# Optimization experiments

Measured on AMD Instinct MI355X. Metric: run time of the kernel, lower is better.

Reference implementation:

```python
import jax, jax.numpy as jnp
import numpy as np

B, P, K = 32, 2048, 16
NHID, NCLS = 128, 10

def setup_inputs() -> dict:
    key = jax.random.key(0)
    ks = jax.random.split(key, 8)
    def w(k, shape):
        fan_in = shape[0]
        return jax.random.normal(k, shape, jnp.float32) / np.sqrt(fan_in)
    pos = jax.random.normal(ks[0], (B * P, 3), jnp.float32)
    batch = jnp.repeat(jnp.arange(B, dtype=jnp.int32), P)
    return dict(
        pos=pos, batch=batch,
        W1a=w(ks[1], (3 + 3, NHID)), b1a=jnp.zeros((NHID,), jnp.float32),
        W1b=w(ks[2], (NHID, NHID)), b1b=jnp.zeros((NHID,), jnp.float32),
        W2a=w(ks[3], (NHID + 3, NHID)), b2a=jnp.zeros((NHID,), jnp.float32),
        W2b=w(ks[4], (NHID, NHID)), b2b=jnp.zeros((NHID,), jnp.float32),
        Wc=w(ks[5], (NHID, NCLS)), bc=jnp.zeros((NCLS,), jnp.float32),
    )

def _gather(x, idx):
    # x: [B,P,C], idx: [B,P,K] -> [B,P,K,C]
    return jax.vmap(lambda xb, ib: xb[ib])(x, idx)

def _knn(posb):
    # posb: [B,P,3]; k nearest (incl. self, loop=True) per node -> [B,P,K]
    sq = jnp.sum(posb * posb, axis=-1)                      # [B,P]
    d2 = sq[:, :, None] + sq[:, None, :] - 2.0 * jnp.einsum('bpd,bqd->bpq', posb, posb)
    _, nbr = jax.lax.top_k(-d2, K)                          # [B,P,K]
    return nbr

def _pointnet_layer(h, posb, nbr, Wa, ba, Wb, bb):
    # message: concat(h_j, pos_j - pos_i) -> Linear -> ReLU -> Linear; aggr = max over K
    h_j = _gather(h, nbr)                                   # [B,P,K,C]
    rel = _gather(posb, nbr) - posb[:, :, None, :]          # [B,P,K,3]
    m = jnp.concatenate([h_j, rel], axis=-1)                # [B,P,K,C+3]
    m = jax.nn.relu(jnp.einsum('bpkc,cd->bpkd', m, Wa) + ba)
    m = jnp.einsum('bpkc,cd->bpkd', m, Wb) + bb
    return jnp.max(m, axis=2)                               # [B,P,NHID]

def reference(pos, batch, W1a, b1a, W1b, b1b, W2a, b2a, W2b, b2b, Wc, bc):
    posb = pos.reshape(B, P, 3)                             # batch is sorted, equal-size graphs
    nbr = _knn(posb)
    h = jax.nn.relu(_pointnet_layer(posb, posb, nbr, W1a, b1a, W1b, b1b))
    h = jax.nn.relu(_pointnet_layer(h, posb, nbr, W2a, b2a, W2b, b2b))
    g = jnp.max(h, axis=1)                                  # global_max_pool -> [B,NHID]
    return g @ Wc + bc                                      # [B,NCLS]
```

## Files before the change

kernel.cpp:

```cpp
#include <hip/hip_runtime.h>


typedef __bf16 bf16x8 __attribute__((ext_vector_type(8)));
typedef float  f32x4  __attribute__((ext_vector_type(4)));

#define LDSA __attribute__((aligned(16)))
#define WAVE_LDS_SYNC() __asm__ volatile("s_waitcnt lgkmcnt(0)" ::: "memory")

__global__ __launch_bounds__(512, 4) void knn_kernel(const float* __restrict__ pos,
                                                     int* __restrict__ nbr) {
  __shared__ LDSA float4 P4[2048];
  const int blk = blockIdx.x;
  const int b = blk >> 5;
  const int tid = threadIdx.x;
  const size_t bbase = (size_t)b * 2048;
  for (int idx = tid; idx < 2048; idx += 512) {
    const float* pp = pos + (bbase + idx) * 3;
    float x = pp[0], y = pp[1], z = pp[2];
    P4[idx] = make_float4(x, y, z, fmaf(z, z, fmaf(y, y, x * x)));
  }
  __syncthreads();
  const int wave = tid >> 6, lane = tid & 63;
  const int p0 = (blk & 31) * 64 + wave * 8;
  const unsigned long long below = (1ull << lane) - 1ull;
  const float FINF = __uint_as_float(0x7F800000u);
  for (int it = 0; it < 8; ++it) {
    const int pl = p0 + it;
    const float4 P = P4[pl];
    float m1 = FINF, m2 = FINF, m3 = FINF, m4 = FINF;
    unsigned s1 = 0, s2 = 0;
#pragma unroll 8
    for (int i = 0; i < 32; ++i) {
      int c = lane + (i << 6);
      float4 Q = P4[c];
      float d2 = (P.w + Q.w) - 2.0f * fmaf(P.z, Q.z, fmaf(P.y, Q.y, P.x * Q.x));
      bool c1 = d2 < m1, c2 = d2 < m2;
      float nm4 = __builtin_amdgcn_fmed3f(m3, m4, d2);
      float nm3 = __builtin_amdgcn_fmed3f(m2, m3, d2);
      float nm2 = __builtin_amdgcn_fmed3f(m1, m2, d2);
      float nm1 = fminf(m1, d2);
      s2 = c1 ? s1 : (c2 ? (unsigned)c : s2);
      s1 = c1 ? (unsigned)c : s1;
      m1 = nm1; m2 = nm2; m3 = nm3; m4 = nm4;
    }
    unsigned k1 = __float_as_uint(m1); k1 = ((int)k1 < 0) ? ~k1 : (k1 | 0x80000000u);
    unsigned k2 = __float_as_uint(m2); k2 = ((int)k2 < 0) ? ~k2 : (k2 | 0x80000000u);
    unsigned k3 = __float_as_uint(m3); k3 = ((int)k3 < 0) ? ~k3 : (k3 | 0x80000000u);
    unsigned k4 = __float_as_uint(m4); k4 = ((int)k4 < 0) ? ~k4 : (k4 | 0x80000000u);
    unsigned v = 0;
#pragma unroll
    for (int bit = 31; bit >= 0; --bit) {
      unsigned t = v | (1u << bit);
      int cnt = __popcll(__ballot(k1 < t)) + __popcll(__ballot(k2 < t)) +
                __popcll(__ballot(k3 < t));
      if (cnt < 16) v = t;
    }
    const unsigned V = v;
    unsigned s3 = 0;
    if (__any(k3 <= V)) {
      const unsigned m3b = __float_as_uint(m3);
#pragma unroll 8
      for (int i = 0; i < 32; ++i) {
        int c = lane + (i << 6);
        float4 Q = P4[c];
        float d2 = (P.w + Q.w) - 2.0f * fmaf(P.z, Q.z, fmaf(P.y, Q.y, P.x * Q.x));
        if (__float_as_uint(d2) == m3b) s3 = (unsigned)c;
      }
    }
    const long long outbase = ((long long)bbase + pl) * 16;
    if (__any(k4 < V)) {
      unsigned long long K1 = ((unsigned long long)k1 << 32) | s1;
      unsigned long long K2 = ((unsigned long long)k2 << 32) | s2;
      unsigned long long K3 = ((unsigned long long)k3 << 32) | s3;
      unsigned long long lastk = 0;
      for (int r = 0; r < 16; ++r) {
        unsigned long long k = K1, kmin = K1;
#pragma unroll
        for (int off = 1; off < 64; off <<= 1) {
          unsigned long long o = __shfl_xor(kmin, off);
          kmin = (o < kmin) ? o : kmin;
        }
        if (lane == r) nbr[outbase + r] = (int)(kmin & 0xFFFFFFFFull);
        if (k == kmin) { lastk = k; K1 = K2; K2 = K3; K3 = ~0ull; }
        if (r < 15 && __any(K1 == ~0ull)) {
          if (K1 == ~0ull) {
            unsigned long long best = ~0ull;
            for (int i = 0; i < 32; ++i) {
              int c = lane + (i << 6);
              float4 Q = P4[c];
              float d2 = (P.w + Q.w) - 2.0f * fmaf(P.z, Q.z, fmaf(P.y, Q.y, P.x * Q.x));
              unsigned u = __float_as_uint(d2);
              u = ((int)u < 0) ? ~u : (u | 0x80000000u);
              unsigned long long kc = ((unsigned long long)u << 32) | (unsigned)c;
              bool ok = (kc > lastk) & (kc < best);
              best = ok ? kc : best;
            }
            K1 = best;
          }
        }
      }
    } else {
      unsigned long long L1 = __ballot(k1 < V), L2 = __ballot(k2 < V), L3 = __ballot(k3 < V);
      unsigned long long E1 = __ballot(k1 == V), E2 = __ballot(k2 == V), E3 = __ballot(k3 == V);
      int cA = __popcll(L1), cB = cA + __popcll(L2), cT = cB + __popcll(L3);
      int eA = __popcll(E1), eB = eA + __popcll(E2);
      {
        bool lt = k1 < V, eq = k1 == V;
        int plt = __popcll(L1 & below);
        int peq = cT + __popcll(E1 & below);
        int p = lt ? plt : peq;
        if (lt || (eq && peq < 16)) nbr[outbase + p] = (int)s1;
      }
      {
        bool lt = k2 < V, eq = k2 == V;
        int plt = cA + __popcll(L2 & below);
        int peq = cT + eA + __popcll(E2 & below);
        int p = lt ? plt : peq;
        if (lt || (eq && peq < 16)) nbr[outbase + p] = (int)s2;
      }
      {
        bool lt = k3 < V, eq = k3 == V;
        int plt = cB + __popcll(L3 & below);
        int peq = cT + eB + __popcll(E3 & below);
        int p = lt ? plt : peq;
        if (lt || (eq && peq < 16)) nbr[outbase + p] = (int)s3;
      }
    }
  }
}

__global__ __launch_bounds__(256, 2) void layer1_kernel(
    const float* __restrict__ pos, const int* __restrict__ nbr,
    const float* __restrict__ W1a, const float* __restrict__ b1a,
    const float* __restrict__ W1b, const float* __restrict__ b1b,
    __bf16* __restrict__ h1e) {
  __shared__ LDSA char smem[52736];
  __bf16* Wbt = (__bf16*)smem;
  const int tid = threadIdx.x;
  for (int idx = tid; idx < 16384; idx += 256) {
    int k = idx >> 7, n = idx & 127;
    int byteoff = n * 256 + ((k * 2) ^ ((n & 7) << 4));
    *(__bf16*)((char*)Wbt + byteoff) = (__bf16)W1b[idx];
  }
  __syncthreads();
  const int wave = tid >> 6, lane = tid & 63;
  const int q = lane >> 4, c15 = lane & 15;
  __bf16* mt = (__bf16*)(smem + 32768) + wave * 2176;
  float* base = (float*)(smem + 50176) + wave * 160;
  const int cb = lane & 7, k0 = lane >> 3, C0 = cb * 16;
  float4 s0h[4], s1h[4], s2h[4];
#pragma unroll
  for (int i = 0; i < 4; ++i) {
    float4 a0 = *(const float4*)&W1a[      C0 + 4 * i], r0 = *(const float4*)&W1a[384 + C0 + 4 * i];
    float4 a1 = *(const float4*)&W1a[128 + C0 + 4 * i], r1 = *(const float4*)&W1a[512 + C0 + 4 * i];
    float4 a2 = *(const float4*)&W1a[256 + C0 + 4 * i], r2 = *(const float4*)&W1a[640 + C0 + 4 * i];
    s0h[i] = make_float4(a0.x + r0.x, a0.y + r0.y, a0.z + r0.z, a0.w + r0.w);
    s1h[i] = make_float4(a1.x + r1.x, a1.y + r1.y, a1.z + r1.z, a1.w + r1.w);
    s2h[i] = make_float4(a2.x + r2.x, a2.y + r2.y, a2.z + r2.z, a2.w + r2.w);
  }
  const int c2 = lane * 2;
  const int bslot = (lane >> 3) * 20 + (lane & 7) * 2;
  const float br0a = W1a[384 + c2], br0b = W1a[384 + c2 + 1];
  const float br1a = W1a[512 + c2], br1b = W1a[512 + c2 + 1];
  const float br2a = W1a[640 + c2], br2b = W1a[640 + c2 + 1];
  const float ba0 = b1a[c2], ba1 = b1a[c2 + 1];
  const float bbi0 = b1b[q * 32 + c15], bbi1 = b1b[q * 32 + 16 + c15];
  const int blk = blockIdx.x, b = blk >> 5;
  const size_t bbase = (size_t)b * 2048;
  const int p0 = (blk & 31) * 64 + wave * 16;
  size_t node = bbase + p0;
  int j0 = nbr[node * 16 + k0];
  int j1 = nbr[node * 16 + k0 + 8];
  float px = pos[node * 3], py = pos[node * 3 + 1], pz = pos[node * 3 + 2];
  for (int it = 0; it < 16; ++it) {
    const int j0c = j0, j1c = j1;
    const float xp = px, yp = py, zp = pz;
    const size_t nodec = node;
    if (it < 15) {
      node = nodec + 1;
      j0 = nbr[node * 16 + k0];
      j1 = nbr[node * 16 + k0 + 8];
      px = pos[node * 3]; py = pos[node * 3 + 1]; pz = pos[node * 3 + 2];
    }
    const float* pj0 = pos + (bbase + j0c) * 3;
    const float* pj1 = pos + (bbase + j1c) * 3;
    const float xa = pj0[0], ya = pj0[1], za = pj0[2];
    const float xb = pj1[0], yb = pj1[1], zb = pj1[2];
    float v0 = ba0 - fmaf(xp, br0a, fmaf(yp, br1a, zp * br2a));
    float v1 = ba1 - fmaf(xp, br0b, fmaf(yp, br1b, zp * br2b));
    *(float2*)&base[bslot] = make_float2(v0, v1);
    WAVE_LDS_SYNC();
    float4 bb[4];
#pragma unroll
    for (int i = 0; i < 4; ++i) bb[i] = *(const float4*)&base[cb * 20 + 4 * i];
#pragma unroll
    for (int r = 0; r < 2; ++r) {
      const float xj = r ? xb : xa, yj = r ? yb : ya, zj = r ? zb : za;
      bf16x8 o0, o1;
#pragma unroll
      for (int i = 0; i < 4; ++i) {
        float mx = fmaf(xj, s0h[i].x, fmaf(yj, s1h[i].x, fmaf(zj, s2h[i].x, bb[i].x)));
        float my = fmaf(xj, s0h[i].y, fmaf(yj, s1h[i].y, fmaf(zj, s2h[i].y, bb[i].y)));
        float mz = fmaf(xj, s0h[i].z, fmaf(yj, s1h[i].z, fmaf(zj, s2h[i].z, bb[i].z)));
        float mw = fmaf(xj, s0h[i].w, fmaf(yj, s1h[i].w, fmaf(zj, s2h[i].w, bb[i].w)));
        __bf16 e0 = (__bf16)fmaxf(mx, 0.f), e1 = (__bf16)fmaxf(my, 0.f);
        __bf16 e2 = (__bf16)fmaxf(mz, 0.f), e3 = (__bf16)fmaxf(mw, 0.f);
        if (i < 2) { o0[i * 4 + 0] = e0; o0[i * 4 + 1] = e1; o0[i * 4 + 2] = e2; o0[i * 4 + 3] = e3; }
        else { o1[(i - 2) * 4 + 0] = e0; o1[(i - 2) * 4 + 1] = e1; o1[(i - 2) * 4 + 2] = e2; o1[(i - 2) * 4 + 3] = e3; }
      }
      __bf16* dst = &mt[(k0 + 8 * r) * 136 + C0];
      *(bf16x8*)dst = o0;
      *(bf16x8*)(dst + 8) = o1;
    }
    WAVE_LDS_SYNC();
    bf16x8 af[4];
#pragma unroll
    for (int t = 0; t < 4; ++t)
      af[t] = *(const bf16x8*)&mt[c15 * 136 + t * 32 + q * 8];
    f32x4 acc[8] = {};
#pragma unroll
    for (int nt = 0; nt < 8; ++nt)
#pragma unroll
      for (int t = 0; t < 4; ++t) {
        const int row = nt * 16 + c15;
        bf16x8 bf = *(const bf16x8*)((const char*)Wbt +
                     row * 256 + (((t * 32 + q * 8) * 2) ^ ((row & 7) << 4)));
        acc[nt] = __builtin_amdgcn_mfma_f32_16x16x32_bf16(af[t], bf, acc[nt], 0, 0, 0);
      }
#pragma unroll
    for (int nt = 0; nt < 8; ++nt) {
      float m4 = fmaxf(fmaxf(acc[nt][0], acc[nt][1]), fmaxf(acc[nt][2], acc[nt][3]));
      m4 = fmaxf(m4, __shfl_xor(m4, 16));
      m4 = fmaxf(m4, __shfl_xor(m4, 32));
      if ((nt >> 1) == q) {
        float bias = (nt & 1) ? bbi1 : bbi0;
        h1e[nodec * 160 + nt * 16 + c15] = (__bf16)fmaxf(m4 + bias, 0.f);
      }
    }
    if (lane < 32) {
      __bf16 v = (__bf16)0.f;
      if (lane == 0) v = (__bf16)xp;
      else if (lane == 1) v = (__bf16)yp;
      else if (lane == 2) v = (__bf16)zp;
      h1e[nodec * 160 + 128 + lane] = v;
    }
  }
}

__global__ __launch_bounds__(256) void mid_gemm_kernel(
    const __bf16* __restrict__ h1e, const float* __restrict__ W2a,
    const float* __restrict__ b2a, __bf16* __restrict__ u2p) {
  __shared__ LDSA __bf16 Wt[128 * 168];
  const int tid = threadIdx.x;
  uint4 z = make_uint4(0, 0, 0, 0);
  for (int idx = tid; idx < 2688; idx += 256) ((uint4*)Wt)[idx] = z;
  __syncthreads();
  for (int idx = tid; idx < 131 * 32; idx += 256) {
    int k = idx >> 5, c4 = (idx & 31) * 4;
    float4 w = *(const float4*)&W2a[k * 128 + c4];
    Wt[(c4 + 0) * 168 + k] = (__bf16)w.x;
    Wt[(c4 + 1) * 168 + k] = (__bf16)w.y;
    Wt[(c4 + 2) * 168 + k] = (__bf16)w.z;
    Wt[(c4 + 3) * 168 + k] = (__bf16)w.w;
  }
  const int wave = tid >> 6, lane = tid & 63;
  const int q = lane >> 4, c15 = lane & 15;
  float biasr[8];
#pragma unroll
  for (int nt = 0; nt < 8; ++nt) biasr[nt] = b2a[nt * 16 + c15];
  __syncthreads();
  for (int tile = 0; tile < 4; ++tile) {
    const int row0 = blockIdx.x * 256 + tile * 64 + wave * 16;
    bf16x8 af[5];
#pragma unroll
    for (int t = 0; t < 5; ++t)
      af[t] = *(const bf16x8*)(h1e + (size_t)(row0 + c15) * 160 + t * 32 + q * 8);
    f32x4 acc[8] = {};
#pragma unroll
    for (int nt = 0; nt < 8; ++nt)
#pragma unroll
      for (int t = 0; t < 5; ++t) {
        bf16x8 bf = *(const bf16x8*)&Wt[(nt * 16 + c15) * 168 + t * 32 + q * 8];
        acc[nt] = __builtin_amdgcn_mfma_f32_16x16x32_bf16(af[t], bf, acc[nt], 0, 0, 0);
      }
#pragma unroll
    for (int nt = 0; nt < 8; ++nt) {
#pragma unroll
      for (int r = 0; r < 4; ++r)
        u2p[(size_t)(row0 + q * 4 + r) * 128 + nt * 16 + c15] = (__bf16)(acc[nt][r] + biasr[nt]);
    }
  }
}

__global__ __launch_bounds__(256, 2) void layer2_kernel(
    const float* __restrict__ pos, const int* __restrict__ nbr,
    const __bf16* __restrict__ u2p, const float* __restrict__ W2a,
    const float* __restrict__ W2b, const float* __restrict__ b2b,
    int* __restrict__ gG) {
  __shared__ LDSA char smem[52736];
  __shared__ int gpart[128];
  __bf16* Wbt = (__bf16*)smem;
  const int tid = threadIdx.x;
  for (int idx = tid; idx < 16384; idx += 256) {
    int k = idx >> 7, n = idx & 127;
    int byteoff = n * 256 + ((k * 2) ^ ((n & 7) << 4));
    *(__bf16*)((char*)Wbt + byteoff) = (__bf16)W2b[idx];
  }
  if (tid < 128) gpart[tid] = 0;
  __syncthreads();
  const int wave = tid >> 6, lane = tid & 63;
  const int q = lane >> 4, c15 = lane & 15;
  __bf16* mt = (__bf16*)(smem + 32768) + wave * 2176;
  float* proj = (float*)(smem + 50176) + wave * 160;
  const int cb = lane & 7, k0 = lane >> 3, C0 = cb * 16;
  const int c2 = lane * 2;
  const int bslot = (lane >> 3) * 20 + (lane & 7) * 2;
  const float r0a = W2a[16384 + c2], r0b = W2a[16384 + c2 + 1];
  const float r1a = W2a[16512 + c2], r1b = W2a[16512 + c2 + 1];
  const float r2a = W2a[16640 + c2], r2b = W2a[16640 + c2 + 1];
  const float bbi0 = b2b[q * 32 + c15], bbi1 = b2b[q * 32 + 16 + c15];
  const int lb = blockIdx.x;
  const int xcd = lb & 7, slot = lb >> 3;
  const int b = xcd + 8 * (slot >> 5);
  const int bi = slot & 31;
  const size_t bbase = (size_t)b * 2048;
  const int p0 = bi * 64 + wave * 16;
  size_t node = bbase + p0;
  int j0 = nbr[node * 16 + k0];
  int j1 = nbr[node * 16 + k0 + 8];
  float px = pos[node * 3], py = pos[node * 3 + 1], pz = pos[node * 3 + 2];
  for (int it = 0; it < 16; ++it) {
    const int j0c = j0, j1c = j1;
    const float xp = px, yp = py, zp = pz;
    const size_t nodec = node;
    if (it < 15) {
      node = nodec + 1;
      j0 = nbr[node * 16 + k0];
      j1 = nbr[node * 16 + k0 + 8];
      px = pos[node * 3]; py = pos[node * 3 + 1]; pz = pos[node * 3 + 2];
    }
    const __bf16* ur0 = u2p + (size_t)(bbase + j0c) * 128 + C0;
    const __bf16* ur1 = u2p + (size_t)(bbase + j1c) * 128 + C0;
    bf16x8 ua0 = *(const bf16x8*)ur0, ua1 = *(const bf16x8*)(ur0 + 8);
    bf16x8 ub0 = *(const bf16x8*)ur1, ub1 = *(const bf16x8*)(ur1 + 8);
    float v0 = fmaf(xp, r0a, fmaf(yp, r1a, zp * r2a));
    float v1 = fmaf(xp, r0b, fmaf(yp, r1b, zp * r2b));
    *(float2*)&proj[bslot] = make_float2(v0, v1);
    WAVE_LDS_SYNC();
    float pj[16];
#pragma unroll
    for (int i = 0; i < 4; ++i) *(float4*)&pj[4 * i] = *(const float4*)&proj[cb * 20 + 4 * i];
#pragma unroll
    for (int r = 0; r < 2; ++r) {
      bf16x8 u0 = r ? ub0 : ua0, u1 = r ? ub1 : ua1;
      bf16x8 o0, o1;
#pragma unroll
      for (int e = 0; e < 8; ++e) o0[e] = (__bf16)fmaxf((float)u0[e] - pj[e], 0.f);
#pragma unroll
      for (int e = 0; e < 8; ++e) o1[e] = (__bf16)fmaxf((float)u1[e] - pj[8 + e], 0.f);
      __bf16* dst = &mt[(k0 + 8 * r) * 136 + C0];
      *(bf16x8*)dst = o0;
      *(bf16x8*)(dst + 8) = o1;
    }
    WAVE_LDS_SYNC();
    bf16x8 af[4];
#pragma unroll
    for (int t = 0; t < 4; ++t)
      af[t] = *(const bf16x8*)&mt[c15 * 136 + t * 32 + q * 8];
    f32x4 acc[8] = {};
#pragma unroll
    for (int nt = 0; nt < 8; ++nt)
#pragma unroll
      for (int t = 0; t < 4; ++t) {
        const int row = nt * 16 + c15;
        bf16x8 bf = *(const bf16x8*)((const char*)Wbt +
                     row * 256 + (((t * 32 + q * 8) * 2) ^ ((row & 7) << 4)));
        acc[nt] = __builtin_amdgcn_mfma_f32_16x16x32_bf16(af[t], bf, acc[nt], 0, 0, 0);
      }
#pragma unroll
    for (int nt = 0; nt < 8; ++nt) {
      float m4 = fmaxf(fmaxf(acc[nt][0], acc[nt][1]), fmaxf(acc[nt][2], acc[nt][3]));
      m4 = fmaxf(m4, __shfl_xor(m4, 16));
      m4 = fmaxf(m4, __shfl_xor(m4, 32));
      if ((nt >> 1) == q) {
        float bias = (nt & 1) ? bbi1 : bbi0;
        float h = fmaxf(m4 + bias, 0.f);
        atomicMax(&gpart[nt * 16 + c15], __float_as_int(h));
      }
    }
  }
  __syncthreads();
  if (tid < 128) atomicMax(&gG[b * 128 + tid], gpart[tid]);
}

__global__ __launch_bounds__(64) void cls_kernel(const int* __restrict__ gG,
                                                 const float* __restrict__ Wc,
                                                 const float* __restrict__ bc,
                                                 float* __restrict__ out) {
  const int b = blockIdx.x, lane = threadIdx.x;
  float g1 = __int_as_float(gG[b * 128 + lane]);
  float g2 = __int_as_float(gG[b * 128 + 64 + lane]);
  float accn[10];
#pragma unroll
  for (int n = 0; n < 10; ++n)
    accn[n] = g1 * Wc[lane * 10 + n] + g2 * Wc[(64 + lane) * 10 + n];
#pragma unroll
  for (int n = 0; n < 10; ++n) {
#pragma unroll
    for (int off = 32; off >= 1; off >>= 1) accn[n] += __shfl_xor(accn[n], off);
  }
  if (lane == 0) {
#pragma unroll
    for (int n = 0; n < 10; ++n) out[b * 10 + n] = accn[n] + bc[n];
  }
}

extern "C" void kernel_launch(void* const* d_in, const int* in_sizes, int n_in,
                              void* d_out, int out_size, void* d_ws, size_t ws_size,
                              hipStream_t stream) {
  const float* pos = (const float*)d_in[0];
  const float* W1a = (const float*)d_in[2];
  const float* b1a = (const float*)d_in[3];
  const float* W1b = (const float*)d_in[4];
  const float* b1b = (const float*)d_in[5];
  const float* W2a = (const float*)d_in[6];
  const float* b2a = (const float*)d_in[7];
  const float* W2b = (const float*)d_in[8];
  const float* b2b = (const float*)d_in[9];
  const float* Wc  = (const float*)d_in[10];
  const float* bc  = (const float*)d_in[11];

  char* ws = (char*)d_ws;
  int*    nbr = (int*)ws;
  __bf16* h1e = (__bf16*)(ws + 4194304);
  __bf16* u2p = (__bf16*)(ws + 25165824);
  int*    gG  = (int*)(ws + 41943040);
  float*  out = (float*)d_out;

  hipMemsetAsync(gG, 0, 32 * 128 * sizeof(int), stream);
  knn_kernel<<<1024, 512, 0, stream>>>(pos, nbr);
  layer1_kernel<<<1024, 256, 0, stream>>>(pos, nbr, W1a, b1a, W1b, b1b, h1e);
  mid_gemm_kernel<<<256, 256, 0, stream>>>(h1e, W2a, b2a, u2p);
  layer2_kernel<<<1024, 256, 0, stream>>>(pos, nbr, u2p, W2a, W2b, b2b, gG);
  cls_kernel<<<32, 64, 0, stream>>>(gG, Wc, bc, out);
}
```

Baseline: 341.4 us.

## Fuse mid GEMM into layer1 epilogue and prefetch layer2 neighbor gathers

The separate mid_gemm kernel is removed. Layer1 now keeps its per-block h1 tile in LDS and, at the end, reloads W2a into the freed LDS region and computes u2p directly, which drops the h1e round trip through global memory and one launch. Layer2 also software-pipelines the u2p neighbor gathers one iteration ahead. In exchange, LDS use in layer1 grows to about 74KB, which may lower occupancy below the 2-block launch bound, and W2a is re-staged once per block.

```diff
diff --git a/kernel.cpp b/kernel.cpp
--- a/kernel.cpp
+++ b/kernel.cpp
@@ -133,8 +133,9 @@
     const float* __restrict__ pos, const int* __restrict__ nbr,
     const float* __restrict__ W1a, const float* __restrict__ b1a,
     const float* __restrict__ W1b, const float* __restrict__ b1b,
-    __bf16* __restrict__ h1e) {
-  __shared__ LDSA char smem[52736];
+    const float* __restrict__ W2a, const float* __restrict__ b2a,
+    __bf16* __restrict__ u2p) {
+  __shared__ LDSA char smem[74240];
   __bf16* Wbt = (__bf16*)smem;
   const int tid = threadIdx.x;
   for (int idx = tid; idx < 16384; idx += 256) {
@@ -147,6 +148,7 @@
   const int q = lane >> 4, c15 = lane & 15;
   __bf16* mt = (__bf16*)(smem + 32768) + wave * 2176;
   float* base = (float*)(smem + 50176) + wave * 160;
+  __bf16* h1t = (__bf16*)(smem + 52736);
   const int cb = lane & 7, k0 = lane >> 3, C0 = cb * 16;
   float4 s0h[4], s1h[4], s2h[4];
 #pragma unroll
@@ -168,7 +170,8 @@
   const int blk = blockIdx.x, b = blk >> 5;
   const size_t bbase = (size_t)b * 2048;
   const int p0 = (blk & 31) * 64 + wave * 16;
-  size_t node = bbase + p0;
+  const size_t row0 = bbase + p0;
+  size_t node = row0;
   int j0 = nbr[node * 16 + k0];
   int j1 = nbr[node * 16 + k0 + 8];
   float px = pos[node * 3], py = pos[node * 3 + 1], pz = pos[node * 3 + 2];
@@ -176,6 +179,7 @@
     const int j0c = j0, j1c = j1;
     const float xp = px, yp = py, zp = pz;
     const size_t nodec = node;
+    const int rl = wave * 16 + it;
     if (it < 15) {
       node = nodec + 1;
       j0 = nbr[node * 16 + k0];
@@ -234,7 +238,7 @@
       m4 = fmaxf(m4, __shfl_xor(m4, 32));
       if ((nt >> 1) == q) {
         float bias = (nt & 1) ? bbi1 : bbi0;
-        h1e[nodec * 160 + nt * 16 + c15] = (__bf16)fmaxf(m4 + bias, 0.f);
+        h1t[rl * 168 + nt * 16 + c15] = (__bf16)fmaxf(m4 + bias, 0.f);
       }
     }
     if (lane < 32) {
@@ -242,53 +246,51 @@
       if (lane == 0) v = (__bf16)xp;
       else if (lane == 1) v = (__bf16)yp;
       else if (lane == 2) v = (__bf16)zp;
-      h1e[nodec * 160 + 128 + lane] = v;
-    }
-  }
-}
-
-__global__ __launch_bounds__(256) void mid_gemm_kernel(
-    const __bf16* __restrict__ h1e, const float* __restrict__ W2a,
-    const float* __restrict__ b2a, __bf16* __restrict__ u2p) {
-  __shared__ LDSA __bf16 Wt[128 * 168];
-  const int tid = threadIdx.x;
-  uint4 z = make_uint4(0, 0, 0, 0);
-  for (int idx = tid; idx < 2688; idx += 256) ((uint4*)Wt)[idx] = z;
-  __syncthreads();
-  for (int idx = tid; idx < 131 * 32; idx += 256) {
+      h1t[rl * 168 + 128 + lane] = v;
+    }
+  }
+  __syncthreads();
+  for (int idx = tid; idx < 4096; idx += 256) {
     int k = idx >> 5, c4 = (idx & 31) * 4;
     float4 w = *(const float4*)&W2a[k * 128 + c4];
-    Wt[(c4 + 0) * 168 + k] = (__bf16)w.x;
-    Wt[(c4 + 1) * 168 + k] = (__bf16)w.y;
-    Wt[(c4 + 2) * 168 + k] = (__bf16)w.z;
-    Wt[(c4 + 3) * 168 + k] = (__bf16)w.w;
-  }
-  const int wave = tid >> 6, lane = tid & 63;
-  const int q = lane >> 4, c15 = lane & 15;
+    *(__bf16*)((char*)smem + (c4 + 0) * 256 + ((k * 2) ^ (((c4 + 0) & 7) << 4))) = (__bf16)w.x;
+    *(__bf16*)((char*)smem + (c4 + 1) * 256 + ((k * 2) ^ (((c4 + 1) & 7) << 4))) = (__bf16)w.y;
+    *(__bf16*)((char*)smem + (c4 + 2) * 256 + ((k * 2) ^ (((c4 + 2) & 7) << 4))) = (__bf16)w.z;
+    *(__bf16*)((char*)smem + (c4 + 3) * 256 + ((k * 2) ^ (((c4 + 3) & 7) << 4))) = (__bf16)w.w;
+  }
+  char* Whi = (char*)smem + 32768;
+  for (int idx = tid; idx < 2560; idx += 256) ((unsigned*)Whi)[idx] = 0u;
+  __syncthreads();
+  for (int idx = tid; idx < 384; idx += 256) {
+    int kk = idx >> 7, n = idx & 127;
+    *(__bf16*)(Whi + n * 80 + kk * 2) = (__bf16)W2a[(128 + kk) * 128 + n];
+  }
+  __syncthreads();
   float biasr[8];
 #pragma unroll
   for (int nt = 0; nt < 8; ++nt) biasr[nt] = b2a[nt * 16 + c15];
-  __syncthreads();
-  for (int tile = 0; tile < 4; ++tile) {
-    const int row0 = blockIdx.x * 256 + tile * 64 + wave * 16;
-    bf16x8 af[5];
-#pragma unroll
-    for (int t = 0; t < 5; ++t)
-      af[t] = *(const bf16x8*)(h1e + (size_t)(row0 + c15) * 160 + t * 32 + q * 8);
-    f32x4 acc[8] = {};
-#pragma unroll
-    for (int nt = 0; nt < 8; ++nt)
-#pragma unroll
-      for (int t = 0; t < 5; ++t) {
-        bf16x8 bf = *(const bf16x8*)&Wt[(nt * 16 + c15) * 168 + t * 32 + q * 8];
-        acc[nt] = __builtin_amdgcn_mfma_f32_16x16x32_bf16(af[t], bf, acc[nt], 0, 0, 0);
-      }
-#pragma unroll
-    for (int nt = 0; nt < 8; ++nt) {
-#pragma unroll
-      for (int r = 0; r < 4; ++r)
-        u2p[(size_t)(row0 + q * 4 + r) * 128 + nt * 16 + c15] = (__bf16)(acc[nt][r] + biasr[nt]);
-    }
+  bf16x8 af2[5];
+#pragma unroll
+  for (int t = 0; t < 5; ++t)
+    af2[t] = *(const bf16x8*)&h1t[(wave * 16 + c15) * 168 + t * 32 + q * 8];
+  f32x4 acc2[8] = {};
+#pragma unroll
+  for (int nt = 0; nt < 8; ++nt) {
+    const int row = nt * 16 + c15;
+#pragma unroll
+    for (int t = 0; t < 4; ++t) {
+      bf16x8 bf = *(const bf16x8*)((const char*)smem +
+                   row * 256 + (((t * 32 + q * 8) * 2) ^ ((row & 7) << 4)));
+      acc2[nt] = __builtin_amdgcn_mfma_f32_16x16x32_bf16(af2[t], bf, acc2[nt], 0, 0, 0);
+    }
+    bf16x8 bf4 = *(const bf16x8*)(Whi + row * 80 + q * 16);
+    acc2[nt] = __builtin_amdgcn_mfma_f32_16x16x32_bf16(af2[4], bf4, acc2[nt], 0, 0, 0);
+  }
+#pragma unroll
+  for (int nt = 0; nt < 8; ++nt) {
+#pragma unroll
+    for (int r = 0; r < 4; ++r)
+      u2p[(row0 + q * 4 + r) * 128 + nt * 16 + c15] = (__bf16)(acc2[nt][r] + biasr[nt]);
   }
 }
 
@@ -329,8 +331,11 @@
   int j0 = nbr[node * 16 + k0];
   int j1 = nbr[node * 16 + k0 + 8];
   float px = pos[node * 3], py = pos[node * 3 + 1], pz = pos[node * 3 + 2];
+  const __bf16* u0p = u2p + (size_t)(bbase + j0) * 128 + C0;
+  const __bf16* u1p = u2p + (size_t)(bbase + j1) * 128 + C0;
+  bf16x8 ua0 = *(const bf16x8*)u0p, ua1 = *(const bf16x8*)(u0p + 8);
+  bf16x8 ub0 = *(const bf16x8*)u1p, ub1 = *(const bf16x8*)(u1p + 8);
   for (int it = 0; it < 16; ++it) {
-    const int j0c = j0, j1c = j1;
     const float xp = px, yp = py, zp = pz;
     const size_t nodec = node;
     if (it < 15) {
@@ -339,10 +344,6 @@
       j1 = nbr[node * 16 + k0 + 8];
       px = pos[node * 3]; py = pos[node * 3 + 1]; pz = pos[node * 3 + 2];
     }
-    const __bf16* ur0 = u2p + (size_t)(bbase + j0c) * 128 + C0;
-    const __bf16* ur1 = u2p + (size_t)(bbase + j1c) * 128 + C0;
-    bf16x8 ua0 = *(const bf16x8*)ur0, ua1 = *(const bf16x8*)(ur0 + 8);
-    bf16x8 ub0 = *(const bf16x8*)ur1, ub1 = *(const bf16x8*)(ur1 + 8);
     float v0 = fmaf(xp, r0a, fmaf(yp, r1a, zp * r2a));
     float v1 = fmaf(xp, r0b, fmaf(yp, r1b, zp * r2b));
     *(float2*)&proj[bslot] = make_float2(v0, v1);
@@ -361,6 +362,12 @@
       __bf16* dst = &mt[(k0 + 8 * r) * 136 + C0];
       *(bf16x8*)dst = o0;
       *(bf16x8*)(dst + 8) = o1;
+    }
+    if (it < 15) {
+      const __bf16* g0 = u2p + (size_t)(bbase + j0) * 128 + C0;
+      const __bf16* g1 = u2p + (size_t)(bbase + j1) * 128 + C0;
+      ua0 = *(const bf16x8*)g0; ua1 = *(const bf16x8*)(g0 + 8);
+      ub0 = *(const bf16x8*)g1; ub1 = *(const bf16x8*)(g1 + 8);
     }
     WAVE_LDS_SYNC();
     bf16x8 af[4];
@@ -432,15 +439,13 @@
 
   char* ws = (char*)d_ws;
   int*    nbr = (int*)ws;
-  __bf16* h1e = (__bf16*)(ws + 4194304);
   __bf16* u2p = (__bf16*)(ws + 25165824);
   int*    gG  = (int*)(ws + 41943040);
   float*  out = (float*)d_out;
 
   hipMemsetAsync(gG, 0, 32 * 128 * sizeof(int), stream);
   knn_kernel<<<1024, 512, 0, stream>>>(pos, nbr);
-  layer1_kernel<<<1024, 256, 0, stream>>>(pos, nbr, W1a, b1a, W1b, b1b, h1e);
-  mid_gemm_kernel<<<256, 256, 0, stream>>>(h1e, W2a, b2a, u2p);
+  layer1_kernel<<<1024, 256, 0, stream>>>(pos, nbr, W1a, b1a, W1b, b1b, W2a, b2a, u2p);
   layer2_kernel<<<1024, 256, 0, stream>>>(pos, nbr, u2p, W2a, W2b, b2b, gG);
   cls_kernel<<<32, 64, 0, stream>>>(gG, Wc, bc, out);
 }
```

New measurement: 343.6 us. About the same (+0.6%).
